# Kernel optimization log

Hardware: AMD Instinct MI355X
Metric: run time of the kernel (lower is better)

## Reference

```python
import jax, jax.numpy as jnp
import numpy as np
from jax import lax

N = 512       # encoder channels
B = 128       # bottleneck channels
K = 3         # depthwise kernel
NUM_BLOCKS = 8
NUM_REPEATS = 3
NUM_SPK = 2
NBLK = NUM_BLOCKS * NUM_REPEATS  # 24
DILATIONS = [2 ** i for i in range(NUM_BLOCKS)] * NUM_REPEATS
EPS = 1e-5


def setup_inputs() -> dict:
    key = jax.random.key(0)
    ks = jax.random.split(key, 12)
    b, L = 4, 8000
    x = jax.random.normal(ks[0], (b, N, L), dtype=jnp.float32)
    # outer GroupNorm affine
    gn_g = 1.0 + 0.05 * jax.random.normal(ks[1], (N,), dtype=jnp.float32)
    gn_b = 0.05 * jax.random.normal(ks[2], (N,), dtype=jnp.float32)
    # 1x1 compression N->B
    w_comp = 0.05 * jax.random.normal(ks[3], (B, N), dtype=jnp.float32)
    # per-block params stacked on leading axis
    dw_w = 0.1 * jax.random.normal(ks[4], (NBLK, B, 1, K), dtype=jnp.float32)   # depthwise weights
    pr_a = 0.25 * jnp.ones((NBLK, B), dtype=jnp.float32) + 0.01 * jax.random.normal(ks[5], (NBLK, B), dtype=jnp.float32)
    tn_g = 1.0 + 0.05 * jax.random.normal(ks[6], (NBLK, B), dtype=jnp.float32)
    tn_b = 0.05 * jax.random.normal(ks[7], (NBLK, B), dtype=jnp.float32)
    pw_w = 0.08 * jax.random.normal(ks[8], (NBLK, B, B), dtype=jnp.float32)     # pointwise 1x1
    # 1x1 expansion B -> N*num_speakers
    w_exp = 0.05 * jax.random.normal(ks[9], (N * NUM_SPK, B), dtype=jnp.float32)
    return {"x": x, "gn_g": gn_g, "gn_b": gn_b, "w_comp": w_comp,
            "dw_w": dw_w, "pr_a": pr_a, "tn_g": tn_g, "tn_b": tn_b,
            "pw_w": pw_w, "w_exp": w_exp}


def _gnorm1(h, g, b):
    # GroupNorm(1, C): normalize over (C, L) per sample, per-channel affine
    m = jnp.mean(h, axis=(1, 2), keepdims=True)
    v = jnp.mean((h - m) ** 2, axis=(1, 2), keepdims=True)
    return (h - m) * lax.rsqrt(v + EPS) * g[None, :, None] + b[None, :, None]


def reference(x, gn_g, gn_b, w_comp, dw_w, pr_a, tn_g, tn_b, pw_w, w_exp):
    out = _gnorm1(x, gn_g, gn_b)                         # [b, N, L]
    out = jnp.einsum('on,bnl->bol', w_comp, out)          # [b, B, L]
    for i in range(NBLK):
        d = DILATIONS[i]
        res = out
        pad_L = (K - 1) * d
        h = jnp.pad(out, ((0, 0), (0, 0), (pad_L, 0)))    # causal left pad
        h = lax.conv_general_dilated(
            h, dw_w[i], window_strides=(1,), padding='VALID',
            rhs_dilation=(d,), dimension_numbers=('NCH', 'OIH', 'NCH'),
            feature_group_count=B)                        # depthwise dilated conv
        a = pr_a[i][None, :, None]
        h = jnp.where(h > 0, h, a * h)                    # PReLU
        h = _gnorm1(h, tn_g[i], tn_b[i])
        h = jnp.einsum('oc,bcl->bol', pw_w[i], h)         # 1x1 pointwise
        out = h + res
    out = jnp.einsum('oc,bcl->bol', w_exp, out)           # [b, N*spk, L]
    out = jax.nn.sigmoid(out)
    b, _, L = out.shape
    return out.reshape(b, NUM_SPK, N, L)
```

## Files before the change

kernel.cpp:

```cpp
#include <hip/hip_runtime.h>
#include <hip/hip_bf16.h>
#include <math.h>
#include <cstddef>

#define LSEQ 8000
#define EPS 1e-5f

typedef unsigned short ushort_t;
typedef __attribute__((ext_vector_type(8))) short s16x8;
typedef __attribute__((ext_vector_type(4))) float f32x4;

__device__ __forceinline__ ushort_t f2bf(float f) {
    union { float f; unsigned u; } x; x.f = f;
    unsigned r = x.u + 0x7FFFu + ((x.u >> 16) & 1u);
    return (ushort_t)(r >> 16);
}

__global__ void cvt_bf16_kernel(const float* __restrict__ src, ushort_t* __restrict__ dst, int n) {
    for (int i = blockIdx.x * blockDim.x + threadIdx.x; i < n; i += gridDim.x * blockDim.x)
        dst[i] = f2bf(src[i]);
}

template<bool DW>
__global__ void stats_kernel(const float* __restrict__ in,
                             const float* __restrict__ dw,
                             const float* __restrict__ pa,
                             int dil, int C,
                             float* __restrict__ stats)
{
    int b = blockIdx.y;
    const float* base = in + (size_t)b * C * LSEQ;
    float s = 0.f, sq = 0.f;
    size_t total = (size_t)C * LSEQ;
    for (size_t idx = (size_t)blockIdx.x * blockDim.x + threadIdx.x; idx < total;
         idx += (size_t)gridDim.x * blockDim.x) {
        float v;
        if (DW) {
            int c = (int)(idx / LSEQ);
            int l = (int)(idx % LSEQ);
            const float* row = base + (size_t)c * LSEQ;
            float x2 = row[l];
            float x1 = (l >= dil) ? row[l - dil] : 0.f;
            float x0 = (l >= 2 * dil) ? row[l - 2 * dil] : 0.f;
            float h = fmaf(dw[c * 3 + 0], x0, fmaf(dw[c * 3 + 1], x1, dw[c * 3 + 2] * x2));
            v = h > 0.f ? h : pa[c] * h;
        } else {
            v = base[idx];
        }
        s += v;
        sq += v * v;
    }
    for (int off = 32; off > 0; off >>= 1) {
        s += __shfl_down(s, off, 64);
        sq += __shfl_down(sq, off, 64);
    }
    __shared__ float red[8][2];
    int wid = threadIdx.x >> 6, lane = threadIdx.x & 63;
    if (lane == 0) { red[wid][0] = s; red[wid][1] = sq; }
    __syncthreads();
    if (threadIdx.x == 0) {
        float ts = 0.f, tq = 0.f;
        int nw = blockDim.x >> 6;
        for (int i = 0; i < nw; i++) { ts += red[i][0]; tq += red[i][1]; }
        atomicAdd(&stats[b * 2 + 0], ts);
        atomicAdd(&stats[b * 2 + 1], tq);
    }
}

template<int KTOT, int MM, int MODE, bool HASRES, bool SIG>
__global__ __launch_bounds__(256)
void gemm_mfma(const float* __restrict__ in,
               const ushort_t* __restrict__ Wb,
               const float* __restrict__ stats,
               const float* __restrict__ g,
               const float* __restrict__ bta,
               const float* __restrict__ dw,
               const float* __restrict__ pa,
               int dil,
               const float* __restrict__ res,
               float* __restrict__ outp)
{
    constexpr int NCHUNK = KTOT / 128;
    __shared__ float hs[128 * 64];
    __shared__ float s_l[(MODE != 2) ? KTOT : 1];
    __shared__ float t_l[(MODE != 2) ? KTOT : 1];
    __shared__ float dw_l[(MODE == 1) ? KTOT * 3 : 1];
    __shared__ float pa_l[(MODE == 1) ? KTOT : 1];

    int tid = threadIdx.x;
    int b = blockIdx.z;
    int l0 = blockIdx.x * 64;
    int obase = blockIdx.y * 128;

    if (MODE != 2) {
        float sum = stats[b * 2 + 0], sumsq = stats[b * 2 + 1];
        float denom = 1.f / ((float)KTOT * (float)LSEQ);
        float m = sum * denom;
        float var = sumsq * denom - m * m;
        float rs = rsqrtf(var + EPS);
        for (int c = tid; c < KTOT; c += 256) {
            float sc = rs * g[c];
            s_l[c] = sc;
            t_l[c] = bta[c] - m * sc;
            if (MODE == 1) {
                dw_l[c * 3 + 0] = dw[c * 3 + 0];
                dw_l[c * 3 + 1] = dw[c * 3 + 1];
                dw_l[c * 3 + 2] = dw[c * 3 + 2];
                pa_l[c] = pa[c];
            }
        }
    }

    int wave = tid >> 6;
    int lane = tid & 63;
    int lg = lane >> 4;
    int lr = lane & 15;
    int rowoff = (wave >> 1) * 64;
    int coloff = (wave & 1) * 32;

    f32x4 acc[4][2];
#pragma unroll
    for (int rf = 0; rf < 4; rf++)
#pragma unroll
        for (int cf = 0; cf < 2; cf++)
            acc[rf][cf] = (f32x4){0.f, 0.f, 0.f, 0.f};

    for (int kc = 0; kc < NCHUNK; kc++) {
        int k0 = kc * 128;
        __syncthreads();
        if (MODE == 1) {
#pragma unroll
            for (int t = 0; t < 32; t++) {
                int idx = tid + t * 256;
                int c = idx >> 6;
                int ll = idx & 63;
                int gl = l0 + ll;
                const float* row = in + ((size_t)b * KTOT + k0 + c) * LSEQ;
                float x2 = row[gl];
                float x1 = (gl >= dil) ? row[gl - dil] : 0.f;
                float x0 = (gl >= 2 * dil) ? row[gl - 2 * dil] : 0.f;
                int cc = k0 + c;
                float h = fmaf(dw_l[cc * 3 + 0], x0, fmaf(dw_l[cc * 3 + 1], x1, dw_l[cc * 3 + 2] * x2));
                h = h > 0.f ? h : pa_l[cc] * h;
                int key = (c & 7) ^ (((c >> 3) & 3) << 2);
                hs[c * 64 + (((ll >> 2) ^ key) << 2) + (ll & 3)] = fmaf(s_l[cc], h, t_l[cc]);
            }
        } else {
#pragma unroll
            for (int t = 0; t < 8; t++) {
                int idx = tid + t * 256;
                int c = idx >> 4;
                int l4 = idx & 15;
                const float* row = in + ((size_t)b * KTOT + k0 + c) * LSEQ + l0 + l4 * 4;
                float4 v = *(const float4*)row;
                if (MODE == 0) {
                    float sc = s_l[k0 + c], tc = t_l[k0 + c];
                    v.x = fmaf(sc, v.x, tc);
                    v.y = fmaf(sc, v.y, tc);
                    v.z = fmaf(sc, v.z, tc);
                    v.w = fmaf(sc, v.w, tc);
                }
                int key = (c & 7) ^ (((c >> 3) & 3) << 2);
                *(float4*)&hs[c * 64 + ((l4 ^ key) << 2)] = v;
            }
        }
        __syncthreads();

        int qbase = (coloff >> 2);
#pragma unroll
        for (int ks = 0; ks < 4; ks++) {
            s16x8 afr[4];
#pragma unroll
            for (int rf = 0; rf < 4; rf++) {
                int row = obase + rowoff + rf * 16 + lr;
                afr[rf] = *(const s16x8*)(Wb + (size_t)row * KTOT + k0 + ks * 32 + lg * 8);
            }
#pragma unroll
            for (int cf = 0; cf < 2; cf++) {
                int col = coloff + cf * 16 + lr;
                int q = col >> 2, sub = col & 3;
                s16x8 bfr;
#pragma unroll
                for (int j = 0; j < 8; j++) {
                    int k = ks * 32 + lg * 8 + j;
                    int key = (k & 7) ^ (((k >> 3) & 3) << 2);
                    float v = hs[k * 64 + ((q ^ key) << 2) + sub];
                    bfr[j] = (short)f2bf(v);
                }
#pragma unroll
                for (int rf = 0; rf < 4; rf++)
                    acc[rf][cf] = __builtin_amdgcn_mfma_f32_16x16x32_bf16(afr[rf], bfr, acc[rf][cf], 0, 0, 0);
            }
        }
    }

#pragma unroll
    for (int rf = 0; rf < 4; rf++) {
#pragma unroll
        for (int cf = 0; cf < 2; cf++) {
#pragma unroll
            for (int r = 0; r < 4; r++) {
                int row = obase + rowoff + rf * 16 + lg * 4 + r;
                int col = l0 + coloff + cf * 16 + lr;
                size_t idx = ((size_t)b * MM + row) * LSEQ + col;
                float v = acc[rf][cf][r];
                if (HASRES) v += res[idx];
                if (SIG) v = 1.f / (1.f + __expf(-v));
                outp[idx] = v;
            }
        }
    }
}

extern "C" void kernel_launch(void* const* d_in, const int* in_sizes, int n_in,
                              void* d_out, int out_size, void* d_ws, size_t ws_size,
                              hipStream_t stream) {
    const float* x      = (const float*)d_in[0];
    const float* gn_g   = (const float*)d_in[1];
    const float* gn_b   = (const float*)d_in[2];
    const float* w_comp = (const float*)d_in[3];
    const float* dw_w   = (const float*)d_in[4];
    const float* pr_a   = (const float*)d_in[5];
    const float* tn_g   = (const float*)d_in[6];
    const float* tn_b   = (const float*)d_in[7];
    const float* pw_w   = (const float*)d_in[8];
    const float* w_exp  = (const float*)d_in[9];
    float* out = (float*)d_out;

    const size_t ACT = (size_t)4 * 128 * LSEQ;
    float* bufA = (float*)d_ws;
    float* bufB = bufA + ACT;
    ushort_t* wcb = (ushort_t*)(bufB + ACT);
    ushort_t* pwb = wcb + 128 * 512;
    ushort_t* web = pwb + 24 * 128 * 128;
    float* stats = (float*)(web + 1024 * 128);

    hipMemsetAsync(stats, 0, 25 * 4 * 2 * sizeof(float), stream);

    cvt_bf16_kernel<<<dim3(256), 256, 0, stream>>>(w_comp, wcb, 128 * 512);
    cvt_bf16_kernel<<<dim3(512), 256, 0, stream>>>(pw_w, pwb, 24 * 128 * 128);
    cvt_bf16_kernel<<<dim3(256), 256, 0, stream>>>(w_exp, web, 1024 * 128);

    stats_kernel<false><<<dim3(512, 4), 256, 0, stream>>>(x, nullptr, nullptr, 0, 512, stats);
    gemm_mfma<512, 128, 0, false, false><<<dim3(125, 1, 4), 256, 0, stream>>>(
        x, wcb, stats, gn_g, gn_b, nullptr, nullptr, 0, nullptr, bufA);

    float* cur = bufA;
    float* nxt = bufB;
    for (int i = 0; i < 24; i++) {
        int dil = 1 << (i & 7);
        float* st = stats + (size_t)(1 + i) * 8;
        stats_kernel<true><<<dim3(256, 4), 256, 0, stream>>>(
            cur, dw_w + (size_t)i * 128 * 3, pr_a + (size_t)i * 128, dil, 128, st);
        gemm_mfma<128, 128, 1, true, false><<<dim3(125, 1, 4), 256, 0, stream>>>(
            cur, pwb + (size_t)i * 128 * 128, st, tn_g + (size_t)i * 128, tn_b + (size_t)i * 128,
            dw_w + (size_t)i * 128 * 3, pr_a + (size_t)i * 128, dil, cur, nxt);
        float* tmp = cur; cur = nxt; nxt = tmp;
    }

    gemm_mfma<128, 1024, 2, false, true><<<dim3(125, 8, 4), 256, 0, stream>>>(
        cur, web, nullptr, nullptr, nullptr, nullptr, nullptr, 0, nullptr, out);
}
```

Baseline: 1.741 ms.

## Use split-bf16 (hi/lo) MFMA GEMMs and per-channel vectorized stats kernel

Weights and activations are each split into high and low bf16 parts, and every GEMM step issues three MFMAs (hi*hi, hi*lo, lo*hi) to get close to fp32 accuracy. The LDS tile now holds the bf16 conversions in a k-contiguous swizzled layout, so the B fragments are read with vector loads and no longer converted inside the inner loop. The stats kernel is reworked so each block handles one channel, using float4 loads where the dilation allows. The three-fold MFMA count and doubled weight and LDS traffic add cost, mainly for accuracy.

```diff
diff --git a/kernel.cpp b/kernel.cpp
--- a/kernel.cpp
+++ b/kernel.cpp
@@ -15,53 +15,81 @@
     unsigned r = x.u + 0x7FFFu + ((x.u >> 16) & 1u);
     return (ushort_t)(r >> 16);
 }
-
-__global__ void cvt_bf16_kernel(const float* __restrict__ src, ushort_t* __restrict__ dst, int n) {
-    for (int i = blockIdx.x * blockDim.x + threadIdx.x; i < n; i += gridDim.x * blockDim.x)
-        dst[i] = f2bf(src[i]);
+__device__ __forceinline__ float bf2f(ushort_t h) {
+    union { unsigned u; float f; } x; x.u = ((unsigned)h) << 16;
+    return x.f;
+}
+
+__global__ void cvt_split_kernel(const float* __restrict__ src,
+                                 ushort_t* __restrict__ hi, ushort_t* __restrict__ lo, int n) {
+    for (int i = blockIdx.x * blockDim.x + threadIdx.x; i < n; i += gridDim.x * blockDim.x) {
+        float v = src[i];
+        ushort_t h = f2bf(v);
+        hi[i] = h;
+        lo[i] = f2bf(v - bf2f(h));
+    }
 }
 
 template<bool DW>
-__global__ void stats_kernel(const float* __restrict__ in,
-                             const float* __restrict__ dw,
-                             const float* __restrict__ pa,
-                             int dil, int C,
-                             float* __restrict__ stats)
+__global__ __launch_bounds__(256)
+void stats_kernel(const float* __restrict__ in,
+                  const float* __restrict__ dw,
+                  const float* __restrict__ pa,
+                  int dil, int C,
+                  float* __restrict__ stats)
 {
     int b = blockIdx.y;
-    const float* base = in + (size_t)b * C * LSEQ;
+    int c = blockIdx.x;
+    const float* row = in + ((size_t)b * C + c) * LSEQ;
+    float d0 = 0.f, d1 = 0.f, d2 = 0.f, aslope = 0.f;
+    if (DW) {
+        d0 = dw[c * 3 + 0]; d1 = dw[c * 3 + 1]; d2 = dw[c * 3 + 2];
+        aslope = pa[c];
+    }
     float s = 0.f, sq = 0.f;
-    size_t total = (size_t)C * LSEQ;
-    for (size_t idx = (size_t)blockIdx.x * blockDim.x + threadIdx.x; idx < total;
-         idx += (size_t)gridDim.x * blockDim.x) {
-        float v;
+    for (int l4 = threadIdx.x * 4; l4 < LSEQ; l4 += 256 * 4) {
+        float4 x2 = *(const float4*)(row + l4);
+        float v0, v1, v2, v3;
         if (DW) {
-            int c = (int)(idx / LSEQ);
-            int l = (int)(idx % LSEQ);
-            const float* row = base + (size_t)c * LSEQ;
-            float x2 = row[l];
-            float x1 = (l >= dil) ? row[l - dil] : 0.f;
-            float x0 = (l >= 2 * dil) ? row[l - 2 * dil] : 0.f;
-            float h = fmaf(dw[c * 3 + 0], x0, fmaf(dw[c * 3 + 1], x1, dw[c * 3 + 2] * x2));
-            v = h > 0.f ? h : pa[c] * h;
+            float x1a[4], x0a[4];
+            if (dil >= 4 && l4 >= 2 * dil) {
+                float4 t1 = *(const float4*)(row + l4 - dil);
+                float4 t0 = *(const float4*)(row + l4 - 2 * dil);
+                x1a[0] = t1.x; x1a[1] = t1.y; x1a[2] = t1.z; x1a[3] = t1.w;
+                x0a[0] = t0.x; x0a[1] = t0.y; x0a[2] = t0.z; x0a[3] = t0.w;
+            } else {
+#pragma unroll
+                for (int j = 0; j < 4; j++) {
+                    int l = l4 + j;
+                    x1a[j] = (l >= dil) ? row[l - dil] : 0.f;
+                    x0a[j] = (l >= 2 * dil) ? row[l - 2 * dil] : 0.f;
+                }
+            }
+            float xa[4] = {x2.x, x2.y, x2.z, x2.w};
+#pragma unroll
+            for (int j = 0; j < 4; j++) {
+                float h = fmaf(d0, x0a[j], fmaf(d1, x1a[j], d2 * xa[j]));
+                h = h > 0.f ? h : aslope * h;
+                xa[j] = h;
+            }
+            v0 = xa[0]; v1 = xa[1]; v2 = xa[2]; v3 = xa[3];
         } else {
-            v = base[idx];
-        }
-        s += v;
-        sq += v * v;
+            v0 = x2.x; v1 = x2.y; v2 = x2.z; v3 = x2.w;
+        }
+        s += v0 + v1 + v2 + v3;
+        sq += v0 * v0 + v1 * v1 + v2 * v2 + v3 * v3;
     }
     for (int off = 32; off > 0; off >>= 1) {
         s += __shfl_down(s, off, 64);
         sq += __shfl_down(sq, off, 64);
     }
-    __shared__ float red[8][2];
+    __shared__ float red[4][2];
     int wid = threadIdx.x >> 6, lane = threadIdx.x & 63;
     if (lane == 0) { red[wid][0] = s; red[wid][1] = sq; }
     __syncthreads();
     if (threadIdx.x == 0) {
-        float ts = 0.f, tq = 0.f;
-        int nw = blockDim.x >> 6;
-        for (int i = 0; i < nw; i++) { ts += red[i][0]; tq += red[i][1]; }
+        float ts = red[0][0] + red[1][0] + red[2][0] + red[3][0];
+        float tq = red[0][1] + red[1][1] + red[2][1] + red[3][1];
         atomicAdd(&stats[b * 2 + 0], ts);
         atomicAdd(&stats[b * 2 + 1], tq);
     }
@@ -70,7 +98,8 @@
 template<int KTOT, int MM, int MODE, bool HASRES, bool SIG>
 __global__ __launch_bounds__(256)
 void gemm_mfma(const float* __restrict__ in,
-               const ushort_t* __restrict__ Wb,
+               const ushort_t* __restrict__ WbH,
+               const ushort_t* __restrict__ WbL,
                const float* __restrict__ stats,
                const float* __restrict__ g,
                const float* __restrict__ bta,
@@ -81,7 +110,8 @@
                float* __restrict__ outp)
 {
     constexpr int NCHUNK = KTOT / 128;
-    __shared__ float hs[128 * 64];
+    __shared__ ushort_t hsH[64 * 128];
+    __shared__ ushort_t hsL[64 * 128];
     __shared__ float s_l[(MODE != 2) ? KTOT : 1];
     __shared__ float t_l[(MODE != 2) ? KTOT : 1];
     __shared__ float dw_l[(MODE == 1) ? KTOT * 3 : 1];
@@ -118,6 +148,10 @@
     int rowoff = (wave >> 1) * 64;
     int coloff = (wave & 1) * 32;
 
+    int scol = tid & 63;
+    int sgk0 = (tid >> 6) * 4;
+    int sgl = l0 + scol;
+
     f32x4 acc[4][2];
 #pragma unroll
     for (int rf = 0; rf < 4; rf++)
@@ -128,68 +162,60 @@
     for (int kc = 0; kc < NCHUNK; kc++) {
         int k0 = kc * 128;
         __syncthreads();
-        if (MODE == 1) {
-#pragma unroll
-            for (int t = 0; t < 32; t++) {
-                int idx = tid + t * 256;
-                int c = idx >> 6;
-                int ll = idx & 63;
-                int gl = l0 + ll;
-                const float* row = in + ((size_t)b * KTOT + k0 + c) * LSEQ;
-                float x2 = row[gl];
-                float x1 = (gl >= dil) ? row[gl - dil] : 0.f;
-                float x0 = (gl >= 2 * dil) ? row[gl - 2 * dil] : 0.f;
-                int cc = k0 + c;
-                float h = fmaf(dw_l[cc * 3 + 0], x0, fmaf(dw_l[cc * 3 + 1], x1, dw_l[cc * 3 + 2] * x2));
-                h = h > 0.f ? h : pa_l[cc] * h;
-                int key = (c & 7) ^ (((c >> 3) & 3) << 2);
-                hs[c * 64 + (((ll >> 2) ^ key) << 2) + (ll & 3)] = fmaf(s_l[cc], h, t_l[cc]);
-            }
-        } else {
-#pragma unroll
-            for (int t = 0; t < 8; t++) {
-                int idx = tid + t * 256;
-                int c = idx >> 4;
-                int l4 = idx & 15;
-                const float* row = in + ((size_t)b * KTOT + k0 + c) * LSEQ + l0 + l4 * 4;
-                float4 v = *(const float4*)row;
-                if (MODE == 0) {
-                    float sc = s_l[k0 + c], tc = t_l[k0 + c];
-                    v.x = fmaf(sc, v.x, tc);
-                    v.y = fmaf(sc, v.y, tc);
-                    v.z = fmaf(sc, v.z, tc);
-                    v.w = fmaf(sc, v.w, tc);
+#pragma unroll
+        for (int gi = 0; gi < 4; gi++) {
+            int gk = sgk0 + gi;
+            s16x8 hv, lv;
+#pragma unroll
+            for (int j = 0; j < 8; j++) {
+                int cc = k0 + gk * 8 + j;
+                const float* row = in + ((size_t)b * KTOT + cc) * LSEQ;
+                float v;
+                if (MODE == 1) {
+                    float x2 = row[sgl];
+                    float x1 = (sgl >= dil) ? row[sgl - dil] : 0.f;
+                    float x0 = (sgl >= 2 * dil) ? row[sgl - 2 * dil] : 0.f;
+                    float h = fmaf(dw_l[cc * 3 + 0], x0,
+                              fmaf(dw_l[cc * 3 + 1], x1, dw_l[cc * 3 + 2] * x2));
+                    h = h > 0.f ? h : pa_l[cc] * h;
+                    v = fmaf(s_l[cc], h, t_l[cc]);
+                } else if (MODE == 0) {
+                    v = fmaf(s_l[cc], row[sgl], t_l[cc]);
+                } else {
+                    v = row[sgl];
                 }
-                int key = (c & 7) ^ (((c >> 3) & 3) << 2);
-                *(float4*)&hs[c * 64 + ((l4 ^ key) << 2)] = v;
-            }
+                ushort_t hb = f2bf(v);
+                hv[j] = (short)hb;
+                lv[j] = (short)f2bf(v - bf2f(hb));
+            }
+            int dst = scol * 128 + ((gk ^ (scol & 7)) << 3);
+            *(s16x8*)&hsH[dst] = hv;
+            *(s16x8*)&hsL[dst] = lv;
         }
         __syncthreads();
 
-        int qbase = (coloff >> 2);
 #pragma unroll
         for (int ks = 0; ks < 4; ks++) {
-            s16x8 afr[4];
+            s16x8 aH[4], aL[4];
 #pragma unroll
             for (int rf = 0; rf < 4; rf++) {
-                int row = obase + rowoff + rf * 16 + lr;
-                afr[rf] = *(const s16x8*)(Wb + (size_t)row * KTOT + k0 + ks * 32 + lg * 8);
+                size_t off = (size_t)(obase + rowoff + rf * 16 + lr) * KTOT + k0 + ks * 32 + lg * 8;
+                aH[rf] = *(const s16x8*)(WbH + off);
+                aL[rf] = *(const s16x8*)(WbL + off);
             }
 #pragma unroll
             for (int cf = 0; cf < 2; cf++) {
                 int col = coloff + cf * 16 + lr;
-                int q = col >> 2, sub = col & 3;
-                s16x8 bfr;
-#pragma unroll
-                for (int j = 0; j < 8; j++) {
-                    int k = ks * 32 + lg * 8 + j;
-                    int key = (k & 7) ^ (((k >> 3) & 3) << 2);
-                    float v = hs[k * 64 + ((q ^ key) << 2) + sub];
-                    bfr[j] = (short)f2bf(v);
+                int gk = ks * 4 + lg;
+                int src = col * 128 + ((gk ^ (col & 7)) << 3);
+                s16x8 bH = *(const s16x8*)&hsH[src];
+                s16x8 bL = *(const s16x8*)&hsL[src];
+#pragma unroll
+                for (int rf = 0; rf < 4; rf++) {
+                    acc[rf][cf] = __builtin_amdgcn_mfma_f32_16x16x32_bf16(aH[rf], bH, acc[rf][cf], 0, 0, 0);
+                    acc[rf][cf] = __builtin_amdgcn_mfma_f32_16x16x32_bf16(aH[rf], bL, acc[rf][cf], 0, 0, 0);
+                    acc[rf][cf] = __builtin_amdgcn_mfma_f32_16x16x32_bf16(aL[rf], bH, acc[rf][cf], 0, 0, 0);
                 }
-#pragma unroll
-                for (int rf = 0; rf < 4; rf++)
-                    acc[rf][cf] = __builtin_amdgcn_mfma_f32_16x16x32_bf16(afr[rf], bfr, acc[rf][cf], 0, 0, 0);
             }
         }
     }
@@ -230,34 +256,38 @@
     const size_t ACT = (size_t)4 * 128 * LSEQ;
     float* bufA = (float*)d_ws;
     float* bufB = bufA + ACT;
-    ushort_t* wcb = (ushort_t*)(bufB + ACT);
-    ushort_t* pwb = wcb + 128 * 512;
-    ushort_t* web = pwb + 24 * 128 * 128;
-    float* stats = (float*)(web + 1024 * 128);
+    ushort_t* wcbH = (ushort_t*)(bufB + ACT);
+    ushort_t* wcbL = wcbH + 128 * 512;
+    ushort_t* pwbH = wcbL + 128 * 512;
+    ushort_t* pwbL = pwbH + 24 * 128 * 128;
+    ushort_t* webH = pwbL + 24 * 128 * 128;
+    ushort_t* webL = webH + 1024 * 128;
+    float* stats = (float*)(webL + 1024 * 128);
 
     hipMemsetAsync(stats, 0, 25 * 4 * 2 * sizeof(float), stream);
 
-    cvt_bf16_kernel<<<dim3(256), 256, 0, stream>>>(w_comp, wcb, 128 * 512);
-    cvt_bf16_kernel<<<dim3(512), 256, 0, stream>>>(pw_w, pwb, 24 * 128 * 128);
-    cvt_bf16_kernel<<<dim3(256), 256, 0, stream>>>(w_exp, web, 1024 * 128);
+    cvt_split_kernel<<<dim3(256), 256, 0, stream>>>(w_comp, wcbH, wcbL, 128 * 512);
+    cvt_split_kernel<<<dim3(512), 256, 0, stream>>>(pw_w, pwbH, pwbL, 24 * 128 * 128);
+    cvt_split_kernel<<<dim3(256), 256, 0, stream>>>(w_exp, webH, webL, 1024 * 128);
 
     stats_kernel<false><<<dim3(512, 4), 256, 0, stream>>>(x, nullptr, nullptr, 0, 512, stats);
     gemm_mfma<512, 128, 0, false, false><<<dim3(125, 1, 4), 256, 0, stream>>>(
-        x, wcb, stats, gn_g, gn_b, nullptr, nullptr, 0, nullptr, bufA);
+        x, wcbH, wcbL, stats, gn_g, gn_b, nullptr, nullptr, 0, nullptr, bufA);
 
     float* cur = bufA;
     float* nxt = bufB;
     for (int i = 0; i < 24; i++) {
         int dil = 1 << (i & 7);
         float* st = stats + (size_t)(1 + i) * 8;
-        stats_kernel<true><<<dim3(256, 4), 256, 0, stream>>>(
+        stats_kernel<true><<<dim3(128, 4), 256, 0, stream>>>(
             cur, dw_w + (size_t)i * 128 * 3, pr_a + (size_t)i * 128, dil, 128, st);
         gemm_mfma<128, 128, 1, true, false><<<dim3(125, 1, 4), 256, 0, stream>>>(
-            cur, pwb + (size_t)i * 128 * 128, st, tn_g + (size_t)i * 128, tn_b + (size_t)i * 128,
+            cur, pwbH + (size_t)i * 128 * 128, pwbL + (size_t)i * 128 * 128, st,
+            tn_g + (size_t)i * 128, tn_b + (size_t)i * 128,
             dw_w + (size_t)i * 128 * 3, pr_a + (size_t)i * 128, dil, cur, nxt);
         float* tmp = cur; cur = nxt; nxt = tmp;
     }
 
     gemm_mfma<128, 1024, 2, false, true><<<dim3(125, 8, 4), 256, 0, stream>>>(
-        cur, web, nullptr, nullptr, nullptr, nullptr, nullptr, 0, nullptr, out);
-}
+        cur, webH, webL, nullptr, nullptr, nullptr, nullptr, nullptr, 0, nullptr, out);
+}
```

Result: faster. 1.567 ms (-10.0%).
